# Optimization experiments

Measured on AMD Instinct MI355X. Metric: run time of the kernel, lower is better.

Reference implementation:

```python
import jax, jax.numpy as jnp
import numpy as np


def _lstm_layer(x, w_ih, w_hh, b, h0, c0):
    # x: [S, B, H]; w_ih, w_hh: [4H, H]; b: [4H] (b_ih + b_hh combined)
    H = h0.shape[-1]

    def step(carry, xt):
        h, c = carry
        gates = xt @ w_ih.T + h @ w_hh.T + b  # [B, 4H]
        i = jax.nn.sigmoid(gates[:, 0 * H:1 * H])
        f = jax.nn.sigmoid(gates[:, 1 * H:2 * H])
        g = jnp.tanh(gates[:, 2 * H:3 * H])
        o = jax.nn.sigmoid(gates[:, 3 * H:4 * H])
        c = f * c + i * g
        h = o * jnp.tanh(c)
        return (h, c), h

    (_, _), hs = jax.lax.scan(step, (h0, c0), x)
    return hs  # [S, B, H]


def setup_inputs() -> dict:
    key = jax.random.key(0)
    ks = jax.random.split(key, 5)
    S, B, H, L, C = 256, 64, 1024, 2, 10
    return {
        "x_data": jax.random.normal(ks[0], (S, B, H), dtype=jnp.float32),
        "weight": jax.random.normal(ks[1], (L, 2, 4 * H, H), dtype=jnp.float32) * 0.05,
        "bias": jax.random.normal(ks[2], (L, 2, 4 * H), dtype=jnp.float32) * 0.05,
        "fc_w": jax.random.normal(ks[3], (C, H), dtype=jnp.float32) * 0.05,
        "fc_b": jax.random.normal(ks[4], (C,), dtype=jnp.float32) * 0.05,
        "hiddenSize": H,
        "miniBatch": B,
        "seqLength": S,
        "numLayers": L,
    }


def reference(x_data, weight, bias, fc_w, fc_b, hiddenSize, miniBatch, seqLength, numLayers):
    B, H = miniBatch, hiddenSize
    h0 = jnp.zeros((B, H), dtype=x_data.dtype)
    c0 = jnp.zeros((B, H), dtype=x_data.dtype)
    x = x_data
    for layer in range(numLayers):
        w_ih = weight[layer, 0]  # [4H, H]
        w_hh = weight[layer, 1]  # [4H, H]
        b = bias[layer, 0] + bias[layer, 1]  # [4H]
        x = _lstm_layer(x, w_ih, w_hh, b, h0, c0)
    out = x[-1]  # last timestep of top layer: [B, H]
    return out @ fc_w.T + fc_b  # [B, num_classes]
```

## Files before the change

kernel.cpp:

```cpp
#include <hip/hip_runtime.h>
#include <cstdint>
#include <cstddef>

#define S_LEN 256
#define BATCH 64
#define HID   1024
#define GATES 4096
#define NBLK  256
#define FLAG_STRIDE 32

typedef _Float16 h16;
typedef _Float16 h16x8 __attribute__((ext_vector_type(8)));
typedef _Float16 h16x4 __attribute__((ext_vector_type(4)));
typedef float    f32x4 __attribute__((ext_vector_type(4)));

__global__ __launch_bounds__(256)
void xconv_kernel(const float* __restrict__ x, h16* __restrict__ x16)
{
  const int n4 = S_LEN * BATCH * HID / 4;
  const int stride = gridDim.x * 256;
  for (int i = blockIdx.x * 256 + threadIdx.x; i < n4; i += stride) {
    f32x4 v = ((const f32x4*)x)[i];
    h16x4 o;
    o[0] = (h16)v[0]; o[1] = (h16)v[1]; o[2] = (h16)v[2]; o[3] = (h16)v[3];
    ((h16x4*)x16)[i] = o;
  }
}

#define RLOAD(dst, ptr, OFFSTR)                                         \
  asm volatile("global_load_dwordx4 %0, %1, off offset:" OFFSTR " sc1"  \
               : "=&v"(dst) : "v"(ptr) : "memory")

__device__ __forceinline__ void grid_barrier(unsigned* flags, int g, int wg)
{
  __syncthreads();
  const unsigned tgt = (unsigned)(g + 1);
  if (threadIdx.x == 0)
    __hip_atomic_store(&flags[wg * FLAG_STRIDE], tgt,
                       __ATOMIC_RELAXED, __HIP_MEMORY_SCOPE_AGENT);
  if (threadIdx.x < NBLK) {
    while (__hip_atomic_load(&flags[threadIdx.x * FLAG_STRIDE],
                             __ATOMIC_RELAXED, __HIP_MEMORY_SCOPE_AGENT) < tgt) {}
  }
  __syncthreads();
}

__global__ __launch_bounds__(512, 1)
void lstm_persistent(const h16* __restrict__ x16,
                     const float* __restrict__ weight,
                     const float* __restrict__ bias,
                     h16* __restrict__ h0r,
                     h16* __restrict__ h1r,
                     unsigned* __restrict__ flags)
{
  __shared__ h16   wlds[65536];
  __shared__ float plds[8][16][32];

  const int wg    = blockIdx.x;
  const int layer = wg >> 7;
  const int j0    = (wg & 127) * 8;
  const int tid   = threadIdx.x;
  const int wave  = tid >> 6, lane = tid & 63;
  const int l15   = lane & 15, l16 = lane >> 4;

  {
    const float* wsrc = weight + (size_t)layer * 2 * GATES * HID;
    for (int c = tid; c < 8192; c += 512) {
      const int ln = c & 63, s = (c >> 6) & 7, n2 = (c >> 9) & 1, w = c >> 10;
      const int lc  = n2 * 16 + (ln & 15);
      const int col = (lc >> 3) * HID + j0 + (lc & 7);
      const int k   = w * 256 + s * 32 + (ln >> 4) * 8;
      const float* p = wsrc + (k < HID ? (size_t)0 : (size_t)GATES * HID)
                            + (size_t)col * HID + (k & (HID - 1));
      h16x8 v;
#pragma unroll
      for (int e = 0; e < 8; ++e) v[e] = (h16)p[e];
      *(h16x8*)&wlds[(size_t)c * 8] = v;
    }
  }
  float bc[4];
  {
    const int j = tid & 7;
#pragma unroll
    for (int gg = 0; gg < 4; ++gg) {
      const int col = gg * HID + j0 + j;
      bc[gg] = bias[(size_t)layer * 2 * GATES + col] +
               bias[(size_t)layer * 2 * GATES + GATES + col];
    }
  }
  float creg[4] = {0.f, 0.f, 0.f, 0.f};
  __syncthreads();

  for (int g = 0; g <= S_LEN; ++g) {
    const bool active = (layer == 0) ? (g < S_LEN) : (g >= 1);
    if (active) {
      const h16 *Alo, *Ahi;
      h16* Hout;
      if (layer == 0) {
        Alo  = x16 + (size_t)g * (BATCH * HID);
        Ahi  = h0r + (size_t)((g + 1) & 1) * (BATCH * HID);
        Hout = h0r + (size_t)(g & 1) * (BATCH * HID);
      } else {
        Alo  = h0r + (size_t)((g - 1) & 1) * (BATCH * HID);
        Ahi  = h1r + (size_t)(g & 1) * (BATCH * HID);
        Hout = h1r + (size_t)((g - 1) & 1) * (BATCH * HID);
      }
      const h16* Asrc = (wave < 4) ? Alo : Ahi;
      const bool ring = (layer == 1) || (wave >= 4);
      const int kb = (wave & 3) * 256;

      const h16* arow[4];
#pragma unroll
      for (int i = 0; i < 4; ++i)
        arow[i] = Asrc + (size_t)(i * 16 + l15) * HID + kb + l16 * 8;
      const h16* bb = wlds + (size_t)wave * 8192 + lane * 8;

      h16x8 a[8][4];
      if (ring) {
#pragma unroll
        for (int i = 0; i < 4; ++i) {
          RLOAD(a[0][i], arow[i], "0");
          RLOAD(a[1][i], arow[i], "64");
          RLOAD(a[2][i], arow[i], "128");
          RLOAD(a[3][i], arow[i], "192");
          RLOAD(a[4][i], arow[i], "256");
          RLOAD(a[5][i], arow[i], "320");
          RLOAD(a[6][i], arow[i], "384");
          RLOAD(a[7][i], arow[i], "448");
        }
        asm volatile("s_waitcnt vmcnt(0)" ::: "memory");
        __builtin_amdgcn_sched_barrier(0);
      } else {
#pragma unroll
        for (int s = 0; s < 8; ++s)
#pragma unroll
          for (int i = 0; i < 4; ++i)
            a[s][i] = *(const h16x8*)(arow[i] + s * 32);
      }

      f32x4 acc[4][2];
#pragma unroll
      for (int i = 0; i < 4; ++i)
#pragma unroll
        for (int n2 = 0; n2 < 2; ++n2) acc[i][n2] = (f32x4)0.f;

#pragma unroll
      for (int s = 0; s < 8; ++s) {
        const h16x8 b0 = *(const h16x8*)(bb + s * 512);
        const h16x8 b1 = *(const h16x8*)(bb + 4096 + s * 512);
#pragma unroll
        for (int i = 0; i < 4; ++i) {
          acc[i][0] = __builtin_amdgcn_mfma_f32_16x16x32_f16(a[s][i], b0, acc[i][0], 0, 0, 0);
          acc[i][1] = __builtin_amdgcn_mfma_f32_16x16x32_f16(a[s][i], b1, acc[i][1], 0, 0, 0);
        }
      }

#pragma unroll
      for (int i = 0; i < 4; ++i) {
#pragma unroll
        for (int n2 = 0; n2 < 2; ++n2)
#pragma unroll
          for (int q = 0; q < 4; ++q) {
            const int r = l16 * 4 + q;
            const int colS = (n2 * 16 + l15) ^ ((r & 7) << 2);
            plds[wave][r][colS] = acc[i][n2][q];
          }
        __syncthreads();
        if (tid < 128) {
          const int r = tid >> 3, j = tid & 7;
          float gv[4];
#pragma unroll
          for (int gg = 0; gg < 4; ++gg) {
            const int colS = (gg * 8 + j) ^ ((r & 7) << 2);
            float s = bc[gg];
#pragma unroll
            for (int w = 0; w < 8; ++w) s += plds[w][r][colS];
            gv[gg] = s;
          }
          const float ig = 1.f / (1.f + __expf(-gv[0]));
          const float fg = 1.f / (1.f + __expf(-gv[1]));
          const float gt = 1.f - 2.f / (__expf(2.f * gv[2]) + 1.f);
          const float og = 1.f / (1.f + __expf(-gv[3]));
          const float cn = fg * creg[i] + ig * gt;
          creg[i] = cn;
          const float th = 1.f - 2.f / (__expf(2.f * cn) + 1.f);
          union { h16 f; unsigned short u; } hb;
          hb.f = (h16)(og * th);
          __hip_atomic_store(
              (unsigned short*)&Hout[(size_t)(i * 16 + r) * HID + j0 + j],
              hb.u, __ATOMIC_RELAXED, __HIP_MEMORY_SCOPE_AGENT);
        }
        __syncthreads();
      }
    }
    grid_barrier(flags, g, wg);
  }
}

__global__ __launch_bounds__(256)
void fc_kernel(const h16* __restrict__ h,
               const float* __restrict__ fw,
               const float* __restrict__ fb,
               float* __restrict__ out)
{
  const int gw = (blockIdx.x * blockDim.x + threadIdx.x) >> 6;
  const int lane = threadIdx.x & 63;
  if (gw >= BATCH * 10) return;
  const int m = gw / 10, cls = gw % 10;
  float s = 0.f;
  for (int k = lane; k < HID; k += 64)
    s += (float)h[(size_t)m * HID + k] * fw[(size_t)cls * HID + k];
#pragma unroll
  for (int off = 32; off; off >>= 1) s += __shfl_down(s, off);
  if (lane == 0) out[m * 10 + cls] = s + fb[cls];
}

extern "C" void kernel_launch(void* const* d_in, const int* in_sizes, int n_in,
                              void* d_out, int out_size, void* d_ws, size_t ws_size,
                              hipStream_t stream)
{
  const float* x      = (const float*)d_in[0];
  const float* weight = (const float*)d_in[1];
  const float* bias   = (const float*)d_in[2];
  const float* fc_w   = (const float*)d_in[3];
  const float* fc_b   = (const float*)d_in[4];
  float* out = (float*)d_out;

  auto align = [](size_t v) { return (v + 255) & ~(size_t)255; };
  const size_t flags_sz = (size_t)NBLK * FLAG_STRIDE * sizeof(unsigned);
  const size_t x16_sz  = (size_t)S_LEN * BATCH * HID * sizeof(h16);
  const size_t ring_sz = (size_t)2 * BATCH * HID * sizeof(h16);

  char* p = (char*)d_ws;
  unsigned* flags = (unsigned*)p; p += align(flags_sz);
  h16* x16 = (h16*)p; p += align(x16_sz);
  h16* h0r = (h16*)p; p += align(ring_sz);
  h16* h1r = (h16*)p; p += align(ring_sz);

  hipMemsetAsync(flags, 0, flags_sz, stream);
  hipMemsetAsync(h0r, 0, ring_sz, stream);
  hipMemsetAsync(h1r, 0, ring_sz, stream);

  xconv_kernel<<<dim3(2048), 256, 0, stream>>>(x, x16);

  lstm_persistent<<<dim3(NBLK), dim3(512), 0, stream>>>(
      x16, weight, bias, h0r, h1r, flags);

  fc_kernel<<<dim3((BATCH * 10 * 64) / 256), 256, 0, stream>>>(
      h1r + (size_t)BATCH * HID, fc_w, fc_b, out);
}
```

Measured before the change: 2.972 ms.

## Replace global grid barrier with per-layer flag dependencies and deeper h0 ring

Drops the all-block grid barrier each step. Each block now waits only on the flags of its own layer's blocks from the previous step and on the other layer's progress. Layer 0 may run up to RING_D steps ahead of layer 1 through a 4-deep h0 ring buffer, which decouples the two layers' pipelines and cuts global synchronization stalls. This adds more complex cross-layer ordering, and with relaxed atomics the correctness of the ring depth and flag checks depends on memory visibility.

```diff
diff --git a/kernel.cpp b/kernel.cpp
--- a/kernel.cpp
+++ b/kernel.cpp
@@ -7,6 +7,7 @@
 #define HID   1024
 #define GATES 4096
 #define NBLK  256
+#define RING_D 4
 #define FLAG_STRIDE 32
 
 typedef _Float16 h16;
@@ -31,20 +32,6 @@
   asm volatile("global_load_dwordx4 %0, %1, off offset:" OFFSTR " sc1"  \
                : "=&v"(dst) : "v"(ptr) : "memory")
 
-__device__ __forceinline__ void grid_barrier(unsigned* flags, int g, int wg)
-{
-  __syncthreads();
-  const unsigned tgt = (unsigned)(g + 1);
-  if (threadIdx.x == 0)
-    __hip_atomic_store(&flags[wg * FLAG_STRIDE], tgt,
-                       __ATOMIC_RELAXED, __HIP_MEMORY_SCOPE_AGENT);
-  if (threadIdx.x < NBLK) {
-    while (__hip_atomic_load(&flags[threadIdx.x * FLAG_STRIDE],
-                             __ATOMIC_RELAXED, __HIP_MEMORY_SCOPE_AGENT) < tgt) {}
-  }
-  __syncthreads();
-}
-
 __global__ __launch_bounds__(512, 1)
 void lstm_persistent(const h16* __restrict__ x16,
                      const float* __restrict__ weight,
@@ -62,6 +49,7 @@
   const int tid   = threadIdx.x;
   const int wave  = tid >> 6, lane = tid & 63;
   const int l15   = lane & 15, l16 = lane >> 4;
+  const int BH    = BATCH * HID;
 
   {
     const float* wsrc = weight + (size_t)layer * 2 * GATES * HID;
@@ -91,109 +79,131 @@
   float creg[4] = {0.f, 0.f, 0.f, 0.f};
   __syncthreads();
 
-  for (int g = 0; g <= S_LEN; ++g) {
-    const bool active = (layer == 0) ? (g < S_LEN) : (g >= 1);
-    if (active) {
-      const h16 *Alo, *Ahi;
-      h16* Hout;
-      if (layer == 0) {
-        Alo  = x16 + (size_t)g * (BATCH * HID);
-        Ahi  = h0r + (size_t)((g + 1) & 1) * (BATCH * HID);
-        Hout = h0r + (size_t)(g & 1) * (BATCH * HID);
-      } else {
-        Alo  = h0r + (size_t)((g - 1) & 1) * (BATCH * HID);
-        Ahi  = h1r + (size_t)(g & 1) * (BATCH * HID);
-        Hout = h1r + (size_t)((g - 1) & 1) * (BATCH * HID);
-      }
-      const h16* Asrc = (wave < 4) ? Alo : Ahi;
-      const bool ring = (layer == 1) || (wave >= 4);
-      const int kb = (wave & 3) * 256;
-
-      const h16* arow[4];
-#pragma unroll
-      for (int i = 0; i < 4; ++i)
-        arow[i] = Asrc + (size_t)(i * 16 + l15) * HID + kb + l16 * 8;
-      const h16* bb = wlds + (size_t)wave * 8192 + lane * 8;
-
-      h16x8 a[8][4];
-      if (ring) {
-#pragma unroll
-        for (int i = 0; i < 4; ++i) {
-          RLOAD(a[0][i], arow[i], "0");
-          RLOAD(a[1][i], arow[i], "64");
-          RLOAD(a[2][i], arow[i], "128");
-          RLOAD(a[3][i], arow[i], "192");
-          RLOAD(a[4][i], arow[i], "256");
-          RLOAD(a[5][i], arow[i], "320");
-          RLOAD(a[6][i], arow[i], "384");
-          RLOAD(a[7][i], arow[i], "448");
+  const int own_base = layer * 128;
+  const int oth_base = (1 - layer) * 128;
+
+  for (int t = 0; t < S_LEN; ++t) {
+    {
+      if (tid < 128) {
+        const unsigned tg = (unsigned)t;
+        if (tg)
+          while (__hip_atomic_load(&flags[(own_base + tid) * FLAG_STRIDE],
+                                   __ATOMIC_RELAXED,
+                                   __HIP_MEMORY_SCOPE_AGENT) < tg) {}
+      } else if (tid < 256) {
+        const int ct = layer ? (t + 1) : (t + 1 - RING_D);
+        if (ct > 0) {
+          const unsigned tg = (unsigned)ct;
+          while (__hip_atomic_load(&flags[(oth_base + tid - 128) * FLAG_STRIDE],
+                                   __ATOMIC_RELAXED,
+                                   __HIP_MEMORY_SCOPE_AGENT) < tg) {}
         }
-        asm volatile("s_waitcnt vmcnt(0)" ::: "memory");
-        __builtin_amdgcn_sched_barrier(0);
-      } else {
-#pragma unroll
-        for (int s = 0; s < 8; ++s)
-#pragma unroll
-          for (int i = 0; i < 4; ++i)
-            a[s][i] = *(const h16x8*)(arow[i] + s * 32);
-      }
-
-      f32x4 acc[4][2];
-#pragma unroll
-      for (int i = 0; i < 4; ++i)
-#pragma unroll
-        for (int n2 = 0; n2 < 2; ++n2) acc[i][n2] = (f32x4)0.f;
-
-#pragma unroll
-      for (int s = 0; s < 8; ++s) {
-        const h16x8 b0 = *(const h16x8*)(bb + s * 512);
-        const h16x8 b1 = *(const h16x8*)(bb + 4096 + s * 512);
-#pragma unroll
-        for (int i = 0; i < 4; ++i) {
-          acc[i][0] = __builtin_amdgcn_mfma_f32_16x16x32_f16(a[s][i], b0, acc[i][0], 0, 0, 0);
-          acc[i][1] = __builtin_amdgcn_mfma_f32_16x16x32_f16(a[s][i], b1, acc[i][1], 0, 0, 0);
+      }
+      __syncthreads();
+    }
+
+    const h16 *Alo, *Ahi;
+    h16* Hout;
+    if (layer == 0) {
+      Alo  = x16 + (size_t)t * BH;
+      Ahi  = h0r + (size_t)((t + RING_D - 1) % RING_D) * BH;
+      Hout = h0r + (size_t)(t % RING_D) * BH;
+    } else {
+      Alo  = h0r + (size_t)(t % RING_D) * BH;
+      Ahi  = h1r + (size_t)((t + 1) & 1) * BH;
+      Hout = h1r + (size_t)(t & 1) * BH;
+    }
+    const h16* Asrc = (wave < 4) ? Alo : Ahi;
+    const bool ring = (layer == 1) || (wave >= 4);
+    const int kb = (wave & 3) * 256;
+
+    const h16* arow[4];
+#pragma unroll
+    for (int i = 0; i < 4; ++i)
+      arow[i] = Asrc + (size_t)(i * 16 + l15) * HID + kb + l16 * 8;
+    const h16* bb = wlds + (size_t)wave * 8192 + lane * 8;
+
+    h16x8 a[8][4];
+    if (ring) {
+#pragma unroll
+      for (int i = 0; i < 4; ++i) {
+        RLOAD(a[0][i], arow[i], "0");
+        RLOAD(a[1][i], arow[i], "64");
+        RLOAD(a[2][i], arow[i], "128");
+        RLOAD(a[3][i], arow[i], "192");
+        RLOAD(a[4][i], arow[i], "256");
+        RLOAD(a[5][i], arow[i], "320");
+        RLOAD(a[6][i], arow[i], "384");
+        RLOAD(a[7][i], arow[i], "448");
+      }
+      asm volatile("s_waitcnt vmcnt(0)" ::: "memory");
+      __builtin_amdgcn_sched_barrier(0);
+    } else {
+#pragma unroll
+      for (int s = 0; s < 8; ++s)
+#pragma unroll
+        for (int i = 0; i < 4; ++i)
+          a[s][i] = *(const h16x8*)(arow[i] + s * 32);
+    }
+
+    f32x4 acc[4][2];
+#pragma unroll
+    for (int i = 0; i < 4; ++i)
+#pragma unroll
+      for (int n2 = 0; n2 < 2; ++n2) acc[i][n2] = (f32x4)0.f;
+
+#pragma unroll
+    for (int s = 0; s < 8; ++s) {
+      const h16x8 b0 = *(const h16x8*)(bb + s * 512);
+      const h16x8 b1 = *(const h16x8*)(bb + 4096 + s * 512);
+#pragma unroll
+      for (int i = 0; i < 4; ++i) {
+        acc[i][0] = __builtin_amdgcn_mfma_f32_16x16x32_f16(a[s][i], b0, acc[i][0], 0, 0, 0);
+        acc[i][1] = __builtin_amdgcn_mfma_f32_16x16x32_f16(a[s][i], b1, acc[i][1], 0, 0, 0);
+      }
+    }
+
+#pragma unroll
+    for (int i = 0; i < 4; ++i) {
+#pragma unroll
+      for (int n2 = 0; n2 < 2; ++n2)
+#pragma unroll
+        for (int q = 0; q < 4; ++q) {
+          const int r = l16 * 4 + q;
+          const int colS = (n2 * 16 + l15) ^ ((r & 7) << 2);
+          plds[wave][r][colS] = acc[i][n2][q];
         }
-      }
-
-#pragma unroll
-      for (int i = 0; i < 4; ++i) {
-#pragma unroll
-        for (int n2 = 0; n2 < 2; ++n2)
-#pragma unroll
-          for (int q = 0; q < 4; ++q) {
-            const int r = l16 * 4 + q;
-            const int colS = (n2 * 16 + l15) ^ ((r & 7) << 2);
-            plds[wave][r][colS] = acc[i][n2][q];
-          }
-        __syncthreads();
-        if (tid < 128) {
-          const int r = tid >> 3, j = tid & 7;
-          float gv[4];
-#pragma unroll
-          for (int gg = 0; gg < 4; ++gg) {
-            const int colS = (gg * 8 + j) ^ ((r & 7) << 2);
-            float s = bc[gg];
-#pragma unroll
-            for (int w = 0; w < 8; ++w) s += plds[w][r][colS];
-            gv[gg] = s;
-          }
-          const float ig = 1.f / (1.f + __expf(-gv[0]));
-          const float fg = 1.f / (1.f + __expf(-gv[1]));
-          const float gt = 1.f - 2.f / (__expf(2.f * gv[2]) + 1.f);
-          const float og = 1.f / (1.f + __expf(-gv[3]));
-          const float cn = fg * creg[i] + ig * gt;
-          creg[i] = cn;
-          const float th = 1.f - 2.f / (__expf(2.f * cn) + 1.f);
-          union { h16 f; unsigned short u; } hb;
-          hb.f = (h16)(og * th);
-          __hip_atomic_store(
-              (unsigned short*)&Hout[(size_t)(i * 16 + r) * HID + j0 + j],
-              hb.u, __ATOMIC_RELAXED, __HIP_MEMORY_SCOPE_AGENT);
+      __syncthreads();
+      if (tid < 128) {
+        const int r = tid >> 3, j = tid & 7;
+        float gv[4];
+#pragma unroll
+        for (int gg = 0; gg < 4; ++gg) {
+          const int colS = (gg * 8 + j) ^ ((r & 7) << 2);
+          float s = bc[gg];
+#pragma unroll
+          for (int w = 0; w < 8; ++w) s += plds[w][r][colS];
+          gv[gg] = s;
         }
-        __syncthreads();
-      }
-    }
-    grid_barrier(flags, g, wg);
+        const float ig = 1.f / (1.f + __expf(-gv[0]));
+        const float fg = 1.f / (1.f + __expf(-gv[1]));
+        const float gt = 1.f - 2.f / (__expf(2.f * gv[2]) + 1.f);
+        const float og = 1.f / (1.f + __expf(-gv[3]));
+        const float cn = fg * creg[i] + ig * gt;
+        creg[i] = cn;
+        const float th = 1.f - 2.f / (__expf(2.f * cn) + 1.f);
+        union { h16 f; unsigned short u; } hb;
+        hb.f = (h16)(og * th);
+        __hip_atomic_store(
+            (unsigned short*)&Hout[(size_t)(i * 16 + r) * HID + j0 + j],
+            hb.u, __ATOMIC_RELAXED, __HIP_MEMORY_SCOPE_AGENT);
+      }
+      __syncthreads();
+    }
+
+    if (tid == 0)
+      __hip_atomic_store(&flags[wg * FLAG_STRIDE], (unsigned)(t + 1),
+                         __ATOMIC_RELAXED, __HIP_MEMORY_SCOPE_AGENT);
   }
 }
 
@@ -228,18 +238,19 @@
 
   auto align = [](size_t v) { return (v + 255) & ~(size_t)255; };
   const size_t flags_sz = (size_t)NBLK * FLAG_STRIDE * sizeof(unsigned);
-  const size_t x16_sz  = (size_t)S_LEN * BATCH * HID * sizeof(h16);
-  const size_t ring_sz = (size_t)2 * BATCH * HID * sizeof(h16);
+  const size_t x16_sz   = (size_t)S_LEN * BATCH * HID * sizeof(h16);
+  const size_t h0r_sz   = (size_t)RING_D * BATCH * HID * sizeof(h16);
+  const size_t h1r_sz   = (size_t)2 * BATCH * HID * sizeof(h16);
 
   char* p = (char*)d_ws;
   unsigned* flags = (unsigned*)p; p += align(flags_sz);
   h16* x16 = (h16*)p; p += align(x16_sz);
-  h16* h0r = (h16*)p; p += align(ring_sz);
-  h16* h1r = (h16*)p; p += align(ring_sz);
+  h16* h0r = (h16*)p; p += align(h0r_sz);
+  h16* h1r = (h16*)p; p += align(h1r_sz);
 
   hipMemsetAsync(flags, 0, flags_sz, stream);
-  hipMemsetAsync(h0r, 0, ring_sz, stream);
-  hipMemsetAsync(h1r, 0, ring_sz, stream);
+  hipMemsetAsync(h0r, 0, h0r_sz, stream);
+  hipMemsetAsync(h1r, 0, h1r_sz, stream);
 
   xconv_kernel<<<dim3(2048), 256, 0, stream>>>(x, x16);
 
```

Measured after the change: 2.900 ms. 2.4% less time.
